# Kernel tuning notes

Hardware: AMD Instinct MI355X
Metric: run time of the kernel (lower is better)

Reference implementation:

```python
import jax, jax.numpy as jnp
import numpy as np

DIM = 2048        # model hidden size
INTER = 1408      # per-expert intermediate size
E = 16            # n_routed_experts
TOPK = 2          # n_activated_experts
S_INTER = 2816    # shared experts intermediate (n_shared_experts * INTER)
T = 4096          # tokens (batch*seq, module flattens to [-1, dim])
ROUTE_SCALE = 1.0


def setup_inputs() -> dict:
    key = jax.random.key(0)
    ks = jax.random.split(key, 8)
    g = lambda k, shape, scale: (jax.random.normal(k, shape, dtype=jnp.float32) * scale)
    return {
        "x": g(ks[0], (T, DIM), 1.0),
        "gate_w": g(ks[1], (E, DIM), 0.02),
        "w1": g(ks[2], (E, INTER, DIM), 0.02),
        "w2": g(ks[3], (E, DIM, INTER), 0.02),
        "w3": g(ks[4], (E, INTER, DIM), 0.02),
        "sw1": g(ks[5], (S_INTER, DIM), 0.02),
        "sw2": g(ks[6], (DIM, S_INTER), 0.02),
        "sw3": g(ks[7], (S_INTER, DIM), 0.02),
    }


def _moe_forward(x, gate_w, w1, w2, w3, sw1, sw2, sw3):
    t = x.shape[0]
    # ---- gate: softmax scores -> top-k experts per token ----
    scores = jax.nn.softmax(x @ gate_w.T, axis=-1)          # [T, E]
    top_w, top_i = jax.lax.top_k(scores, TOPK)              # [T, K]
    top_w = top_w * ROUTE_SCALE
    # dense combine weights [T, E]: zero for unselected experts
    combine = jnp.zeros((t, E), x.dtype).at[jnp.arange(t)[:, None], top_i].add(top_w)
    # ---- routed experts: gated silu MLP per expert, weighted combine ----
    # loop over the small fixed expert count; tokens with combine==0 contribute 0,
    # matching the original scatter/gather dispatch math exactly.
    y = jnp.zeros_like(x)
    for e in range(E):
        h = jax.nn.silu(x @ w1[e].T) * (x @ w3[e].T)        # [T, INTER]
        y = y + (h @ w2[e].T) * combine[:, e:e + 1]
    # ---- shared experts ----
    z = (jax.nn.silu(x @ sw1.T) * (x @ sw3.T)) @ sw2.T      # [T, DIM]
    return y + z


def reference(x, gate_w, w1, w2, w3, sw1, sw2, sw3):
    return _moe_forward(x, gate_w, w1, w2, w3, sw1, sw2, sw3)
```

## Files before the change

kernel.cpp:

```cpp
#include <hip/hip_runtime.h>
#include <hip/hip_bf16.h>
#include <cstdint>
#include <cstddef>

#define TTOK   4096
#define DIM_   2048
#define INTER_ 1408
#define NEXP   16
#define SINTER_ 2816
#define BM 128
#define BN 128
#define BK 32
#define MAXROWS (TTOK*2 + NEXP*BM)
#define MAXMT   (TTOK*2/BM + NEXP)

typedef unsigned short u16;
typedef __attribute__((ext_vector_type(8))) short short8;
typedef __attribute__((ext_vector_type(4))) float f32x4;

__device__ __forceinline__ u16 f2bf(float f) {
    unsigned u = __float_as_uint(f);
    u += 0x7FFFu + ((u >> 16) & 1u);
    return (u16)(u >> 16);
}

__device__ __forceinline__ int4 pack8(float4 a, float4 b) {
    int4 r;
    r.x = (int)f2bf(a.x) | ((int)f2bf(a.y) << 16);
    r.y = (int)f2bf(a.z) | ((int)f2bf(a.w) << 16);
    r.z = (int)f2bf(b.x) | ((int)f2bf(b.y) << 16);
    r.w = (int)f2bf(b.z) | ((int)f2bf(b.w) << 16);
    return r;
}


__global__ void init_kernel(int* perm_rt, float* pw_rt, int* perm_sh, int* misc) {
    int i = blockIdx.x * 256 + threadIdx.x;
    if (i < MAXROWS) { perm_rt[i] = -1; pw_rt[i] = 0.f; }
    if (i < TTOK)    perm_sh[i] = i;
    if (i < 32)      misc[i] = 0;
}

__global__ void convert_x_kernel(const float* __restrict__ x, u16* __restrict__ xb) {
    size_t i = (size_t)blockIdx.x * 256 + threadIdx.x;
    float4 v = *(const float4*)(x + i * 4);
    uint2 o;
    o.x = (unsigned)f2bf(v.x) | ((unsigned)f2bf(v.y) << 16);
    o.y = (unsigned)f2bf(v.z) | ((unsigned)f2bf(v.w) << 16);
    *(uint2*)(xb + i * 4) = o;
}

__global__ void gate_kernel(const float* __restrict__ x, const float* __restrict__ gw,
                            int* __restrict__ topi, float* __restrict__ topw,
                            int* __restrict__ misc) {
    int t = blockIdx.x;
    int lane = threadIdx.x;
    const float* xr = x + (size_t)t * DIM_;
    float acc[NEXP];
#pragma unroll
    for (int e = 0; e < NEXP; e++) acc[e] = 0.f;
#pragma unroll
    for (int i = 0; i < 8; i++) {
        int k = i * 256 + lane * 4;
        float4 xv = *(const float4*)(xr + k);
#pragma unroll
        for (int e = 0; e < NEXP; e++) {
            float4 gv = *(const float4*)(gw + (size_t)e * DIM_ + k);
            acc[e] += xv.x * gv.x + xv.y * gv.y + xv.z * gv.z + xv.w * gv.w;
        }
    }
#pragma unroll
    for (int e = 0; e < NEXP; e++) {
        float v = acc[e];
        for (int off = 32; off > 0; off >>= 1) v += __shfl_down(v, off);
        acc[e] = v;
    }
    if (lane == 0) {
        float m = acc[0];
#pragma unroll
        for (int e = 1; e < NEXP; e++) m = fmaxf(m, acc[e]);
        float p[NEXP]; float s = 0.f;
#pragma unroll
        for (int e = 0; e < NEXP; e++) { p[e] = __expf(acc[e] - m); s += p[e]; }
        int i0 = 0; float v0 = p[0];
#pragma unroll
        for (int e = 1; e < NEXP; e++) if (p[e] > v0) { v0 = p[e]; i0 = e; }
        int i1 = -1; float v1 = -1.f;
#pragma unroll
        for (int e = 0; e < NEXP; e++) if (e != i0 && p[e] > v1) { v1 = p[e]; i1 = e; }
        float inv = 1.f / s;
        topi[2 * t] = i0; topi[2 * t + 1] = i1;
        topw[2 * t] = v0 * inv; topw[2 * t + 1] = v1 * inv;
        atomicAdd(&misc[i0], 1);
        atomicAdd(&misc[i1], 1);
    }
}

__global__ void scan_kernel(int* misc) {
    int* counts = misc;
    int* base   = misc + 32;
    int* te     = misc + 48;
    int* tr     = misc + 128;
    int b = 0, tt = 0;
    for (int e = 0; e < NEXP; e++) {
        int c = counts[e];
        int nt = (c + BM - 1) >> 7;
        base[e] = b;
        for (int i = 0; i < nt; i++) { te[tt] = e; tr[tt] = b + i * BM; tt++; }
        b += nt * BM;
    }
    for (int i = tt; i < MAXMT; i++) te[i] = -1;
}

__global__ void scatter_kernel(const int* __restrict__ topi, const float* __restrict__ topw,
                               int* __restrict__ misc, int* __restrict__ perm,
                               float* __restrict__ pw) {
    int t = blockIdx.x * 256 + threadIdx.x;
    if (t >= TTOK) return;
    int* fill = misc + 16;
    int* base = misc + 32;
#pragma unroll
    for (int k = 0; k < 2; k++) {
        int e = topi[2 * t + k];
        int pos = base[e] + atomicAdd(&fill[e], 1);
        perm[pos] = t;
        pw[pos] = topw[2 * t + k];
    }
}


template<bool GROUPED>
__global__ __launch_bounds__(256, 2) void gemm_h13_k(
    const u16* __restrict__ Xb,
    const float* __restrict__ W1b, const float* __restrict__ W3b,
    u16* __restrict__ H,
    const int* __restrict__ perm,
    const int* __restrict__ te, const int* __restrict__ tr,
    int N, int K)
{
    int e, slot0;
    if (GROUPED) {
        e = te[blockIdx.x];
        if (e < 0) return;
        slot0 = tr[blockIdx.x];
    } else { e = 0; slot0 = blockIdx.x * BM; }
    const int n0 = blockIdx.y * BN;
    const float* W1 = W1b + (size_t)e * N * K;
    const float* W3 = W3b + (size_t)e * N * K;

    __shared__ __align__(16) u16 As[BM * BK];
    __shared__ __align__(16) u16 B1s[BM * BK];
    __shared__ __align__(16) u16 B3s[BM * BK];

    const int tid = threadIdx.x;
    const int lane = tid & 63, wid = tid >> 6;
    const int wr = wid >> 1, wc = wid & 1;
    const int col = lane & 15, kg = lane >> 4;

    const int r0 = tid >> 2, ko = (tid & 3) * 8;
    const int tok0 = perm[slot0 + r0];
    const int tok1 = perm[slot0 + r0 + 64];
    const int rB = tid >> 1, hfB = (tid & 1) * 16;
    const float* p1 = W1 + (size_t)(n0 + rB) * K + hfB;
    const float* p3 = W3 + (size_t)(n0 + rB) * K + hfB;

    f32x4 acc1[4][4] = {};
    f32x4 acc3[4][4] = {};

    for (int k0 = 0; k0 < K; k0 += BK) {
        int4 va0 = make_int4(0, 0, 0, 0), va1 = make_int4(0, 0, 0, 0);
        if (tok0 >= 0) va0 = *(const int4*)(Xb + (size_t)tok0 * K + k0 + ko);
        if (tok1 >= 0) va1 = *(const int4*)(Xb + (size_t)tok1 * K + k0 + ko);
        *(int4*)(As + r0 * BK + ko) = va0;
        *(int4*)(As + (r0 + 64) * BK + ko) = va1;

        float4 a0 = *(const float4*)(p1 + k0);
        float4 a1 = *(const float4*)(p1 + k0 + 4);
        float4 a2 = *(const float4*)(p1 + k0 + 8);
        float4 a3 = *(const float4*)(p1 + k0 + 12);
        *(int4*)(B1s + rB * BK + hfB)     = pack8(a0, a1);
        *(int4*)(B1s + rB * BK + hfB + 8) = pack8(a2, a3);
        float4 c0 = *(const float4*)(p3 + k0);
        float4 c1 = *(const float4*)(p3 + k0 + 4);
        float4 c2 = *(const float4*)(p3 + k0 + 8);
        float4 c3 = *(const float4*)(p3 + k0 + 12);
        *(int4*)(B3s + rB * BK + hfB)     = pack8(c0, c1);
        *(int4*)(B3s + rB * BK + hfB + 8) = pack8(c2, c3);

        __syncthreads();

        short8 a[4];
#pragma unroll
        for (int mi = 0; mi < 4; mi++)
            a[mi] = *(const short8*)(As + (wr * 64 + mi * 16 + col) * BK + kg * 8);
#pragma unroll
        for (int ni = 0; ni < 4; ni++) {
            short8 v1 = *(const short8*)(B1s + (wc * 64 + ni * 16 + col) * BK + kg * 8);
            short8 v3 = *(const short8*)(B3s + (wc * 64 + ni * 16 + col) * BK + kg * 8);
#pragma unroll
            for (int mi = 0; mi < 4; mi++) {
                acc1[mi][ni] = __builtin_amdgcn_mfma_f32_16x16x32_bf16(a[mi], v1, acc1[mi][ni], 0, 0, 0);
                acc3[mi][ni] = __builtin_amdgcn_mfma_f32_16x16x32_bf16(a[mi], v3, acc3[mi][ni], 0, 0, 0);
            }
        }
        __syncthreads();
    }

#pragma unroll
    for (int mi = 0; mi < 4; mi++) {
#pragma unroll
        for (int j = 0; j < 4; j++) {
            int row = slot0 + wr * 64 + mi * 16 + kg * 4 + j;
#pragma unroll
            for (int ni = 0; ni < 4; ni++) {
                float v1 = acc1[mi][ni][j];
                float v3 = acc3[mi][ni][j];
                float hv = v1 / (1.f + __expf(-v1)) * v3;
                int c = n0 + wc * 64 + ni * 16 + col;
                H[(size_t)row * N + c] = f2bf(hv);
            }
        }
    }
}

template<bool ATOMIC>
__global__ __launch_bounds__(256, 2) void gemm_out_k(
    const u16* __restrict__ Hm,
    const float* __restrict__ W2b,
    float* __restrict__ Out,
    const int* __restrict__ perm, const float* __restrict__ pw,
    const int* __restrict__ te, const int* __restrict__ tr,
    int K)
{
    int e, slot0;
    if (ATOMIC) {
        e = te[blockIdx.x];
        if (e < 0) return;
        slot0 = tr[blockIdx.x];
    } else { e = 0; slot0 = blockIdx.x * BM; }
    const int n0 = blockIdx.y * BN;
    const float* W2 = W2b + (size_t)e * DIM_ * K;

    __shared__ __align__(16) u16 As[BM * BK];
    __shared__ __align__(16) u16 Bs[BM * BK];

    const int tid = threadIdx.x;
    const int lane = tid & 63, wid = tid >> 6;
    const int wr = wid >> 1, wc = wid & 1;
    const int col = lane & 15, kg = lane >> 4;

    const int r0 = tid >> 2, ko = (tid & 3) * 8;
    const int rB = tid >> 1, hfB = (tid & 1) * 16;
    const float* p2 = W2 + (size_t)(n0 + rB) * K + hfB;

    f32x4 acc[4][4] = {};

    for (int k0 = 0; k0 < K; k0 += BK) {
        int4 va0 = *(const int4*)(Hm + (size_t)(slot0 + r0) * K + k0 + ko);
        int4 va1 = *(const int4*)(Hm + (size_t)(slot0 + r0 + 64) * K + k0 + ko);
        *(int4*)(As + r0 * BK + ko) = va0;
        *(int4*)(As + (r0 + 64) * BK + ko) = va1;

        float4 a0 = *(const float4*)(p2 + k0);
        float4 a1 = *(const float4*)(p2 + k0 + 4);
        float4 a2 = *(const float4*)(p2 + k0 + 8);
        float4 a3 = *(const float4*)(p2 + k0 + 12);
        *(int4*)(Bs + rB * BK + hfB)     = pack8(a0, a1);
        *(int4*)(Bs + rB * BK + hfB + 8) = pack8(a2, a3);

        __syncthreads();

        short8 a[4];
#pragma unroll
        for (int mi = 0; mi < 4; mi++)
            a[mi] = *(const short8*)(As + (wr * 64 + mi * 16 + col) * BK + kg * 8);
#pragma unroll
        for (int ni = 0; ni < 4; ni++) {
            short8 bv = *(const short8*)(Bs + (wc * 64 + ni * 16 + col) * BK + kg * 8);
#pragma unroll
            for (int mi = 0; mi < 4; mi++)
                acc[mi][ni] = __builtin_amdgcn_mfma_f32_16x16x32_bf16(a[mi], bv, acc[mi][ni], 0, 0, 0);
        }
        __syncthreads();
    }

#pragma unroll
    for (int mi = 0; mi < 4; mi++) {
#pragma unroll
        for (int j = 0; j < 4; j++) {
            int rloc = wr * 64 + mi * 16 + kg * 4 + j;
            int slot = slot0 + rloc;
            if (ATOMIC) {
                int token = perm[slot];
                if (token < 0) continue;
                float w = pw[slot];
#pragma unroll
                for (int ni = 0; ni < 4; ni++) {
                    int c = n0 + wc * 64 + ni * 16 + col;
                    atomicAdd(&Out[(size_t)token * DIM_ + c], acc[mi][ni][j] * w);
                }
            } else {
#pragma unroll
                for (int ni = 0; ni < 4; ni++) {
                    int c = n0 + wc * 64 + ni * 16 + col;
                    Out[(size_t)slot * DIM_ + c] = acc[mi][ni][j];
                }
            }
        }
    }
}


extern "C" void kernel_launch(void* const* d_in, const int* in_sizes, int n_in,
                              void* d_out, int out_size, void* d_ws, size_t ws_size,
                              hipStream_t stream) {
    (void)in_sizes; (void)n_in; (void)out_size; (void)ws_size;
    const float* x   = (const float*)d_in[0];
    const float* gw  = (const float*)d_in[1];
    const float* w1  = (const float*)d_in[2];
    const float* w2  = (const float*)d_in[3];
    const float* w3  = (const float*)d_in[4];
    const float* sw1 = (const float*)d_in[5];
    const float* sw2 = (const float*)d_in[6];
    const float* sw3 = (const float*)d_in[7];
    float* out = (float*)d_out;

    char* ws = (char*)d_ws;
    size_t off = 0;
    auto take = [&](size_t bytes) -> void* {
        void* p = ws + off;
        off += (bytes + 255) & ~(size_t)255;
        return p;
    };
    u16*   xb      = (u16*)take((size_t)TTOK * DIM_ * 2);
    u16*   hbuf    = (u16*)take((size_t)MAXROWS * INTER_ * 2);
    int*   perm_rt = (int*)take((size_t)MAXROWS * 4);
    float* pw_rt   = (float*)take((size_t)MAXROWS * 4);
    int*   perm_sh = (int*)take((size_t)TTOK * 4);
    int*   topi    = (int*)take((size_t)TTOK * 2 * 4);
    float* topw    = (float*)take((size_t)TTOK * 2 * 4);
    int*   misc    = (int*)take(1024);

    init_kernel<<<MAXROWS / 256, 256, 0, stream>>>(perm_rt, pw_rt, perm_sh, misc);
    convert_x_kernel<<<(TTOK * DIM_ / 4) / 256, 256, 0, stream>>>(x, xb);
    gate_kernel<<<TTOK, 64, 0, stream>>>(x, gw, topi, topw, misc);
    scan_kernel<<<1, 1, 0, stream>>>(misc);
    scatter_kernel<<<TTOK / 256, 256, 0, stream>>>(topi, topw, misc, perm_rt, pw_rt);

    gemm_h13_k<false><<<dim3(TTOK / BM, SINTER_ / BN), 256, 0, stream>>>(
        xb, sw1, sw3, hbuf, perm_sh, nullptr, nullptr, SINTER_, DIM_);
    gemm_out_k<false><<<dim3(TTOK / BM, DIM_ / BN), 256, 0, stream>>>(
        hbuf, sw2, out, nullptr, nullptr, nullptr, nullptr, SINTER_);

    gemm_h13_k<true><<<dim3(MAXMT, INTER_ / BN), 256, 0, stream>>>(
        xb, w1, w3, hbuf, perm_rt, misc + 48, misc + 128, INTER_, DIM_);
    gemm_out_k<true><<<dim3(MAXMT, DIM_ / BN), 256, 0, stream>>>(
        hbuf, w2, out, perm_rt, pw_rt, misc + 48, misc + 128, INTER_);
}
```

Before: 988.9 us.

## Prefetch next K tile into registers, remap blocks XCD-aware, use packed bf16 convert

The GEMM main loops now load the next K-slice of activations and fp32 weights into registers right after the barrier, so global-load latency overlaps the MFMA work on the current slice. Launch grids become 1D, and block IDs are remapped so that consecutive blocks landing on the same XCD (blockIdx & 7) cover contiguous M-tiles of the same N-column. This aims to improve L2 reuse of weight tiles. Float-to-bf16 packing switches to the v_cvt_pk_bf16_f32 instruction. The changes add register pressure under launch_bounds(256,2), and grid padding adds a few early-exit blocks.

```diff
diff --git a/kernel.cpp b/kernel.cpp
--- a/kernel.cpp
+++ b/kernel.cpp
@@ -19,17 +19,22 @@
 typedef __attribute__((ext_vector_type(4))) float f32x4;
 
 __device__ __forceinline__ u16 f2bf(float f) {
-    unsigned u = __float_as_uint(f);
-    u += 0x7FFFu + ((u >> 16) & 1u);
-    return (u16)(u >> 16);
+    __hip_bfloat16 h = __float2bfloat16(f);
+    union { __hip_bfloat16 h; u16 u; } c; c.h = h; return c.u;
+}
+
+__device__ __forceinline__ unsigned pk2(float a, float b) {
+    unsigned r;
+    asm("v_cvt_pk_bf16_f32 %0, %1, %2" : "=v"(r) : "v"(a), "v"(b));
+    return r;
 }
 
 __device__ __forceinline__ int4 pack8(float4 a, float4 b) {
     int4 r;
-    r.x = (int)f2bf(a.x) | ((int)f2bf(a.y) << 16);
-    r.y = (int)f2bf(a.z) | ((int)f2bf(a.w) << 16);
-    r.z = (int)f2bf(b.x) | ((int)f2bf(b.y) << 16);
-    r.w = (int)f2bf(b.z) | ((int)f2bf(b.w) << 16);
+    r.x = (int)pk2(a.x, a.y);
+    r.y = (int)pk2(a.z, a.w);
+    r.z = (int)pk2(b.x, b.y);
+    r.w = (int)pk2(b.z, b.w);
     return r;
 }
 
@@ -45,8 +50,8 @@
     size_t i = (size_t)blockIdx.x * 256 + threadIdx.x;
     float4 v = *(const float4*)(x + i * 4);
     uint2 o;
-    o.x = (unsigned)f2bf(v.x) | ((unsigned)f2bf(v.y) << 16);
-    o.y = (unsigned)f2bf(v.z) | ((unsigned)f2bf(v.w) << 16);
+    o.x = pk2(v.x, v.y);
+    o.y = pk2(v.z, v.w);
     *(uint2*)(xb + i * 4) = o;
 }
 
@@ -136,15 +141,15 @@
     u16* __restrict__ H,
     const int* __restrict__ perm,
     const int* __restrict__ te, const int* __restrict__ tr,
-    int N, int K)
+    int N, int K, int nt_m, int chunk)
 {
+    const int q = (blockIdx.x & 7) * chunk + (blockIdx.x >> 3);
+    if (q >= nt_m * (N / BN)) return;
+    const int jn = q / nt_m, im = q % nt_m;
     int e, slot0;
-    if (GROUPED) {
-        e = te[blockIdx.x];
-        if (e < 0) return;
-        slot0 = tr[blockIdx.x];
-    } else { e = 0; slot0 = blockIdx.x * BM; }
-    const int n0 = blockIdx.y * BN;
+    if (GROUPED) { e = te[im]; if (e < 0) return; slot0 = tr[im]; }
+    else         { e = 0; slot0 = im * BM; }
+    const int n0 = jn * BN;
     const float* W1 = W1b + (size_t)e * N * K;
     const float* W3 = W3b + (size_t)e * N * K;
 
@@ -160,6 +165,8 @@
     const int r0 = tid >> 2, ko = (tid & 3) * 8;
     const int tok0 = perm[slot0 + r0];
     const int tok1 = perm[slot0 + r0 + 64];
+    const u16* pA0 = (tok0 >= 0) ? Xb + (size_t)tok0 * K + ko : nullptr;
+    const u16* pA1 = (tok1 >= 0) ? Xb + (size_t)tok1 * K + ko : nullptr;
     const int rB = tid >> 1, hfB = (tid & 1) * 16;
     const float* p1 = W1 + (size_t)(n0 + rB) * K + hfB;
     const float* p3 = W3 + (size_t)(n0 + rB) * K + hfB;
@@ -167,27 +174,33 @@
     f32x4 acc1[4][4] = {};
     f32x4 acc3[4][4] = {};
 
+    int4 va0, va1;
+    float4 f1[4], f3[4];
+
+    va0 = pA0 ? *(const int4*)(pA0) : make_int4(0, 0, 0, 0);
+    va1 = pA1 ? *(const int4*)(pA1) : make_int4(0, 0, 0, 0);
+#pragma unroll
+    for (int i = 0; i < 4; i++) { f1[i] = *(const float4*)(p1 + i * 4); f3[i] = *(const float4*)(p3 + i * 4); }
+
     for (int k0 = 0; k0 < K; k0 += BK) {
-        int4 va0 = make_int4(0, 0, 0, 0), va1 = make_int4(0, 0, 0, 0);
-        if (tok0 >= 0) va0 = *(const int4*)(Xb + (size_t)tok0 * K + k0 + ko);
-        if (tok1 >= 0) va1 = *(const int4*)(Xb + (size_t)tok1 * K + k0 + ko);
         *(int4*)(As + r0 * BK + ko) = va0;
         *(int4*)(As + (r0 + 64) * BK + ko) = va1;
-
-        float4 a0 = *(const float4*)(p1 + k0);
-        float4 a1 = *(const float4*)(p1 + k0 + 4);
-        float4 a2 = *(const float4*)(p1 + k0 + 8);
-        float4 a3 = *(const float4*)(p1 + k0 + 12);
-        *(int4*)(B1s + rB * BK + hfB)     = pack8(a0, a1);
-        *(int4*)(B1s + rB * BK + hfB + 8) = pack8(a2, a3);
-        float4 c0 = *(const float4*)(p3 + k0);
-        float4 c1 = *(const float4*)(p3 + k0 + 4);
-        float4 c2 = *(const float4*)(p3 + k0 + 8);
-        float4 c3 = *(const float4*)(p3 + k0 + 12);
-        *(int4*)(B3s + rB * BK + hfB)     = pack8(c0, c1);
-        *(int4*)(B3s + rB * BK + hfB + 8) = pack8(c2, c3);
-
+        *(int4*)(B1s + rB * BK + hfB)     = pack8(f1[0], f1[1]);
+        *(int4*)(B1s + rB * BK + hfB + 8) = pack8(f1[2], f1[3]);
+        *(int4*)(B3s + rB * BK + hfB)     = pack8(f3[0], f3[1]);
+        *(int4*)(B3s + rB * BK + hfB + 8) = pack8(f3[2], f3[3]);
         __syncthreads();
+
+        const int kn = k0 + BK;
+        if (kn < K) {
+            va0 = pA0 ? *(const int4*)(pA0 + kn) : make_int4(0, 0, 0, 0);
+            va1 = pA1 ? *(const int4*)(pA1 + kn) : make_int4(0, 0, 0, 0);
+#pragma unroll
+            for (int i = 0; i < 4; i++) {
+                f1[i] = *(const float4*)(p1 + kn + i * 4);
+                f3[i] = *(const float4*)(p3 + kn + i * 4);
+            }
+        }
 
         short8 a[4];
 #pragma unroll
@@ -230,15 +243,15 @@
     float* __restrict__ Out,
     const int* __restrict__ perm, const float* __restrict__ pw,
     const int* __restrict__ te, const int* __restrict__ tr,
-    int K)
+    int K, int nt_m, int chunk)
 {
+    const int q = (blockIdx.x & 7) * chunk + (blockIdx.x >> 3);
+    if (q >= nt_m * (DIM_ / BN)) return;
+    const int jn = q / nt_m, im = q % nt_m;
     int e, slot0;
-    if (ATOMIC) {
-        e = te[blockIdx.x];
-        if (e < 0) return;
-        slot0 = tr[blockIdx.x];
-    } else { e = 0; slot0 = blockIdx.x * BM; }
-    const int n0 = blockIdx.y * BN;
+    if (ATOMIC) { e = te[im]; if (e < 0) return; slot0 = tr[im]; }
+    else        { e = 0; slot0 = im * BM; }
+    const int n0 = jn * BN;
     const float* W2 = W2b + (size_t)e * DIM_ * K;
 
     __shared__ __align__(16) u16 As[BM * BK];
@@ -251,24 +264,33 @@
 
     const int r0 = tid >> 2, ko = (tid & 3) * 8;
     const int rB = tid >> 1, hfB = (tid & 1) * 16;
+    const u16* pA0 = Hm + (size_t)(slot0 + r0) * K + ko;
+    const u16* pA1 = Hm + (size_t)(slot0 + r0 + 64) * K + ko;
     const float* p2 = W2 + (size_t)(n0 + rB) * K + hfB;
 
     f32x4 acc[4][4] = {};
 
+    int4 va0, va1;
+    float4 fb[4];
+    va0 = *(const int4*)(pA0);
+    va1 = *(const int4*)(pA1);
+#pragma unroll
+    for (int i = 0; i < 4; i++) fb[i] = *(const float4*)(p2 + i * 4);
+
     for (int k0 = 0; k0 < K; k0 += BK) {
-        int4 va0 = *(const int4*)(Hm + (size_t)(slot0 + r0) * K + k0 + ko);
-        int4 va1 = *(const int4*)(Hm + (size_t)(slot0 + r0 + 64) * K + k0 + ko);
         *(int4*)(As + r0 * BK + ko) = va0;
         *(int4*)(As + (r0 + 64) * BK + ko) = va1;
-
-        float4 a0 = *(const float4*)(p2 + k0);
-        float4 a1 = *(const float4*)(p2 + k0 + 4);
-        float4 a2 = *(const float4*)(p2 + k0 + 8);
-        float4 a3 = *(const float4*)(p2 + k0 + 12);
-        *(int4*)(Bs + rB * BK + hfB)     = pack8(a0, a1);
-        *(int4*)(Bs + rB * BK + hfB + 8) = pack8(a2, a3);
-
+        *(int4*)(Bs + rB * BK + hfB)     = pack8(fb[0], fb[1]);
+        *(int4*)(Bs + rB * BK + hfB + 8) = pack8(fb[2], fb[3]);
         __syncthreads();
+
+        const int kn = k0 + BK;
+        if (kn < K) {
+            va0 = *(const int4*)(pA0 + kn);
+            va1 = *(const int4*)(pA1 + kn);
+#pragma unroll
+            for (int i = 0; i < 4; i++) fb[i] = *(const float4*)(p2 + kn + i * 4);
+        }
 
         short8 a[4];
 #pragma unroll
@@ -347,13 +369,27 @@
     scan_kernel<<<1, 1, 0, stream>>>(misc);
     scatter_kernel<<<TTOK / 256, 256, 0, stream>>>(topi, topw, misc, perm_rt, pw_rt);
 
-    gemm_h13_k<false><<<dim3(TTOK / BM, SINTER_ / BN), 256, 0, stream>>>(
-        xb, sw1, sw3, hbuf, perm_sh, nullptr, nullptr, SINTER_, DIM_);
-    gemm_out_k<false><<<dim3(TTOK / BM, DIM_ / BN), 256, 0, stream>>>(
-        hbuf, sw2, out, nullptr, nullptr, nullptr, nullptr, SINTER_);
-
-    gemm_h13_k<true><<<dim3(MAXMT, INTER_ / BN), 256, 0, stream>>>(
-        xb, w1, w3, hbuf, perm_rt, misc + 48, misc + 128, INTER_, DIM_);
-    gemm_out_k<true><<<dim3(MAXMT, DIM_ / BN), 256, 0, stream>>>(
-        hbuf, w2, out, perm_rt, pw_rt, misc + 48, misc + 128, INTER_);
-}
+    auto grid8 = [](int total) { return ((total + 7) / 8) * 8; };
+    auto chunk8 = [](int total) { return (total + 7) / 8; };
+
+    {
+        int total = (TTOK / BM) * (SINTER_ / BN);
+        gemm_h13_k<false><<<grid8(total), 256, 0, stream>>>(
+            xb, sw1, sw3, hbuf, perm_sh, nullptr, nullptr, SINTER_, DIM_, TTOK / BM, chunk8(total));
+    }
+    {
+        int total = (TTOK / BM) * (DIM_ / BN);
+        gemm_out_k<false><<<grid8(total), 256, 0, stream>>>(
+            hbuf, sw2, out, nullptr, nullptr, nullptr, nullptr, SINTER_, TTOK / BM, chunk8(total));
+    }
+    {
+        int total = MAXMT * (INTER_ / BN);
+        gemm_h13_k<true><<<grid8(total), 256, 0, stream>>>(
+            xb, w1, w3, hbuf, perm_rt, misc + 48, misc + 128, INTER_, DIM_, MAXMT, chunk8(total));
+    }
+    {
+        int total = MAXMT * (DIM_ / BN);
+        gemm_out_k<true><<<grid8(total), 256, 0, stream>>>(
+            hbuf, w2, out, perm_rt, pw_rt, misc + 48, misc + 128, INTER_, MAXMT, chunk8(total));
+    }
+}
```

Measured after the change: 868.7 us. 1.14x faster.
